# Kernel optimization log

Hardware: AMD Instinct MI355X
Metric: run time of the kernel (lower is better)

Reference implementation:

```python
import jax, jax.numpy as jnp
import numpy as np

N_NODES = 100000
N_EDGES = 3200000
HID = 52
N_LAYERS = 3


def setup_inputs() -> dict:
    key = jax.random.key(0)
    ks = jax.random.split(key, 6)
    x = jax.random.normal(ks[0], (N_NODES, HID), dtype=jnp.float32)
    edge_index = jax.random.randint(ks[1], (2, N_EDGES), 0, N_NODES, dtype=jnp.int32)
    w1 = jax.random.normal(ks[2], (N_LAYERS, HID, 2 * HID), dtype=jnp.float32) * 0.1
    b1 = jnp.zeros((N_LAYERS, 2 * HID), dtype=jnp.float32)
    w2 = jax.random.normal(ks[3], (N_LAYERS, 2 * HID, HID), dtype=jnp.float32) * 0.1
    b2 = jnp.zeros((N_LAYERS, HID), dtype=jnp.float32)
    eps = jnp.zeros((N_LAYERS,), dtype=jnp.float32)
    lin_w = jax.random.normal(ks[4], (HID * (N_LAYERS + 1), HID), dtype=jnp.float32) * 0.1
    lin_b = jnp.zeros((HID,), dtype=jnp.float32)
    return {"x": x, "edge_index": edge_index, "w1": w1, "b1": b1,
            "w2": w2, "b2": b2, "eps": eps, "lin_w": lin_w, "lin_b": lin_b}


def reference(x, edge_index, w1, b1, w2, b2, eps, lin_w, lin_b):
    src, dst = edge_index[0], edge_index[1]
    n = x.shape[0]
    h = x
    h_list = [x]
    for l in range(N_LAYERS):
        # GINConv: sum-aggregate neighbor features at target nodes
        agg = jax.ops.segment_sum(h[src], dst, num_segments=n)  # [N, HID]
        z = (1.0 + eps[l]) * h + agg
        # 2-layer MLP: Linear -> ReLU -> Linear
        z = jnp.maximum(z @ w1[l] + b1[l], 0.0) @ w2[l] + b2[l]
        # outer ReLU (dropout p=0 is identity)
        h = jnp.maximum(z, 0.0)
        h_list.append(h)
    node_repr = jnp.concatenate(h_list, axis=1)  # [N, HID*(L+1)]
    return node_repr @ lin_w + lin_b
```

## Files before the change

### kernel.cpp

```cpp
#include <hip/hip_runtime.h>

#define HID 52
#define HID2 104
#define P1_CHUNK 8192
#define NBIN_MAX 512
#define HSTRIDE 136
#define BINCAP 10240
#define SR_STRIDE 14336

typedef unsigned short ushort_t;
typedef unsigned int uint_t;
typedef short bf16x8 __attribute__((ext_vector_type(8)));
typedef float f32x4 __attribute__((ext_vector_type(4)));
typedef float f32x2 __attribute__((ext_vector_type(2)));

__device__ __forceinline__ ushort_t f2bf(float f) {
    union { float f; uint_t u; } c; c.f = f;
    uint_t u = c.u + 0x7FFFu + ((c.u >> 16) & 1u);
    return (ushort_t)(u >> 16);
}
__device__ __forceinline__ float bflo(uint_t u) {
    union { uint_t u; float f; } c; c.u = u << 16; return c.f;
}
__device__ __forceinline__ float bfhi(uint_t u) {
    union { uint_t u; float f; } c; c.u = u & 0xFFFF0000u; return c.f;
}
__device__ __forceinline__ f32x2 rawpair(uint_t a, uint_t b) {
    union { uint_t u; float f; } ca, cb; ca.u = a; cb.u = b;
    return (f32x2){ca.f, cb.f};
}
__device__ __forceinline__ f32x2 shlpair(uint_t a, uint_t b) {
    union { uint_t u; float f; } ca, cb; ca.u = a << 16; cb.u = b << 16;
    return (f32x2){ca.f, cb.f};
}
__device__ __forceinline__ void pkacc(f32x2& a, f32x2 b) {
    asm("v_pk_add_f32 %0, %0, %1" : "+v"(a) : "v"(b));
}
template<int IMM>
__device__ __forceinline__ f32x2 swz2(f32x2 v) {
    union { float f; int i; } a, b; a.f = v.x; b.f = v.y;
    int ra = __builtin_amdgcn_ds_swizzle(a.i, IMM);
    int rb = __builtin_amdgcn_ds_swizzle(b.i, IMM);
    union { int i; float f; } c, d; c.i = ra; d.i = rb;
    return (f32x2){c.f, d.f};
}

__global__ __launch_bounds__(512) void pass1_kernel(const int* __restrict__ src,
                                                    const int* __restrict__ dst,
                                                    int* __restrict__ gcnt,
                                                    uint_t* __restrict__ packed, int E) {
    __shared__ uint_t stage[P1_CHUNK];
    __shared__ ushort_t sbin[P1_CHUNK];
    __shared__ int cnt[NBIN_MAX];
    __shared__ int curs[NBIN_MAX];
    __shared__ int diff[NBIN_MAX];
    __shared__ int wsum[8];
    int tid = threadIdx.x;
    int lane = tid & 63, wv = tid >> 6;
    cnt[tid] = 0;
    __syncthreads();
    int base = blockIdx.x * P1_CHUNK;
    int cend = min(P1_CHUNK, E - base);
    int nq = cend >> 2;
    const uint4* d4p = (const uint4*)(dst + base);
    const uint4* s4p = (const uint4*)(src + base);
    for (int j = tid; j < nq; j += 512) {
        uint4 d = d4p[j];
        atomicAdd(&cnt[d.x >> 8], 1);
        atomicAdd(&cnt[d.y >> 8], 1);
        atomicAdd(&cnt[d.z >> 8], 1);
        atomicAdd(&cnt[d.w >> 8], 1);
    }
    for (int i = (nq << 2) + tid; i < cend; i += 512)
        atomicAdd(&cnt[((uint_t)dst[base + i]) >> 8], 1);
    __syncthreads();
    int c = cnt[tid];
    int inc = c;
#pragma unroll
    for (int off = 1; off < 64; off <<= 1) {
        int t = __shfl_up(inc, off);
        if (lane >= off) inc += t;
    }
    if (lane == 63) wsum[wv] = inc;
    __syncthreads();
    int wpre = 0;
#pragma unroll
    for (int i = 0; i < 7; i++) wpre += (i < wv) ? wsum[i] : 0;
    int ex = wpre + inc - c;
    curs[tid] = ex;
    int g = c ? (tid * BINCAP + atomicAdd(&gcnt[tid], c)) : 0;
    diff[tid] = g - ex;
    __syncthreads();
    for (int j = tid; j < nq; j += 512) {
        uint4 d = d4p[j];
        uint4 s = s4p[j];
        int b, pos;
        b = d.x >> 8; pos = atomicAdd(&curs[b], 1);
        stage[pos] = (s.x << 8) | (d.x & 255u); sbin[pos] = (ushort_t)b;
        b = d.y >> 8; pos = atomicAdd(&curs[b], 1);
        stage[pos] = (s.y << 8) | (d.y & 255u); sbin[pos] = (ushort_t)b;
        b = d.z >> 8; pos = atomicAdd(&curs[b], 1);
        stage[pos] = (s.z << 8) | (d.z & 255u); sbin[pos] = (ushort_t)b;
        b = d.w >> 8; pos = atomicAdd(&curs[b], 1);
        stage[pos] = (s.w << 8) | (d.w & 255u); sbin[pos] = (ushort_t)b;
    }
    for (int i = (nq << 2) + tid; i < cend; i += 512) {
        uint_t d = (uint_t)dst[base + i];
        uint_t s = (uint_t)src[base + i];
        int b = d >> 8;
        int pos = atomicAdd(&curs[b], 1);
        stage[pos] = (s << 8) | (d & 255u);
        sbin[pos] = (ushort_t)b;
    }
    __syncthreads();
    for (int i = tid; i < cend; i += 512) {
        packed[diff[sbin[i]] + i] = stage[i];
    }
}

__global__ __launch_bounds__(256) void mid_kernel(const uint_t* __restrict__ packed,
                                                  const int* __restrict__ gcnt,
                                                  int* __restrict__ srcsorted,
                                                  int* __restrict__ nrs,
                                                  int* __restrict__ ndeg,
                                                  const float* __restrict__ x,
                                                  const float* __restrict__ w1,
                                                  const float* __restrict__ w2,
                                                  const float* __restrict__ lin_w,
                                                  ushort_t* __restrict__ xb,
                                                  ushort_t* __restrict__ h1b,
                                                  ushort_t* __restrict__ h2b,
                                                  ushort_t* __restrict__ w1f,
                                                  ushort_t* __restrict__ w2f,
                                                  ushort_t* __restrict__ linf,
                                                  int N, int nbin, int nconv) {
    __shared__ int hist[256];
    __shared__ int curs[256];
    __shared__ int wsum[4];
    int blk = blockIdx.x;
    int tid = threadIdx.x;
    if (blk < nbin) {
        int b = blk;
        int lane = tid & 63, wv = tid >> 6;
        hist[tid] = 0;
        __syncthreads();
        int beg = b * BINCAP;
        int cntE = gcnt[b];
        int nq = cntE >> 2;
        const uint4* p4p = (const uint4*)(packed + beg);
        for (int j = tid; j < nq; j += 256) {
            uint4 p = p4p[j];
            atomicAdd(&hist[p.x & 255u], 1);
            atomicAdd(&hist[p.y & 255u], 1);
            atomicAdd(&hist[p.z & 255u], 1);
            atomicAdd(&hist[p.w & 255u], 1);
        }
        for (int i = (nq << 2) + tid; i < cntE; i += 256)
            atomicAdd(&hist[packed[beg + i] & 255u], 1);
        __syncthreads();
        int v = hist[tid];
        int pv = (v + 15) & ~15;
        int inc = pv;
#pragma unroll
        for (int off = 1; off < 64; off <<= 1) {
            int t = __shfl_up(inc, off);
            if (lane >= off) inc += t;
        }
        if (lane == 63) wsum[wv] = inc;
        __syncthreads();
        int wpre = 0;
#pragma unroll
        for (int i = 0; i < 3; i++) wpre += (i < wv) ? wsum[i] : 0;
        int start = b * SR_STRIDE + wpre + inc - pv;
        int node = b * 256 + tid;
        if (node < N) { nrs[node] = start; ndeg[node] = pv; }
        curs[tid] = start;
        __syncthreads();
        for (int j = tid; j < nq; j += 256) {
            uint4 p = p4p[j];
            int pos;
            pos = atomicAdd(&curs[p.x & 255u], 1); srcsorted[pos] = (int)(p.x >> 8);
            pos = atomicAdd(&curs[p.y & 255u], 1); srcsorted[pos] = (int)(p.y >> 8);
            pos = atomicAdd(&curs[p.z & 255u], 1); srcsorted[pos] = (int)(p.z >> 8);
            pos = atomicAdd(&curs[p.w & 255u], 1); srcsorted[pos] = (int)(p.w >> 8);
        }
        for (int i = (nq << 2) + tid; i < cntE; i += 256) {
            uint_t p = packed[beg + i];
            int pos = atomicAdd(&curs[p & 255u], 1);
            srcsorted[pos] = (int)(p >> 8);
        }
        __syncthreads();
        for (int i = start + v; i < start + pv; i++) srcsorted[i] = N;
        return;
    }
    if (blk < nbin + nconv) {
        int t = (blk - nbin) * 256 + tid;
        if (t >= N * 8) return;
        int node = t >> 3, pp = t & 7, c0 = pp * 8;
        uint4 u = make_uint4(0, 0, 0, 0);
        if (c0 < 48) {
            float4 xa = *(const float4*)(x + (size_t)node * HID + c0);
            float4 xc = *(const float4*)(x + (size_t)node * HID + c0 + 4);
            u.x = (uint_t)f2bf(xa.x) | ((uint_t)f2bf(xa.y) << 16);
            u.y = (uint_t)f2bf(xa.z) | ((uint_t)f2bf(xa.w) << 16);
            u.z = (uint_t)f2bf(xc.x) | ((uint_t)f2bf(xc.y) << 16);
            u.w = (uint_t)f2bf(xc.z) | ((uint_t)f2bf(xc.w) << 16);
        } else if (c0 == 48) {
            float4 xa = *(const float4*)(x + (size_t)node * HID + 48);
            u.x = (uint_t)f2bf(xa.x) | ((uint_t)f2bf(xa.y) << 16);
            u.y = (uint_t)f2bf(xa.z) | ((uint_t)f2bf(xa.w) << 16);
        }
        *(uint4*)(xb + (size_t)node * 64 + c0) = u;
        return;
    }
    if (blk == nbin + nconv) {
        ushort_t* arr = (tid < 64) ? xb : (tid < 128) ? h1b : h2b;
        arr[(size_t)N * 64 + (tid & 63)] = 0;
        return;
    }
    int gid = (blk - nbin - nconv - 1) * 4 + (tid >> 6);
    int lane = tid & 63;
    if (gid >= 122) return;
    int m = lane & 15, q = lane >> 4;
    ushort_t o[8];
    ushort_t* dstp;
    if (gid < 42) {
        int l = gid / 14, r = gid % 14, ct = r >> 1, ks = r & 1;
        int nn = ct * 16 + m;
#pragma unroll
        for (int j = 0; j < 8; j++) {
            int k = ks * 32 + q * 8 + j;
            o[j] = (k < HID && nn < HID2) ? f2bf(w1[((size_t)l * HID + k) * HID2 + nn]) : 0;
        }
        dstp = w1f + ((size_t)(l * 14 + ct * 2 + ks) * 64 + lane) * 8;
    } else if (gid < 90) {
        int g2 = gid - 42, l = g2 / 16, r = g2 % 16, ct = r >> 2, ks = r & 3;
        int nn = ct * 16 + m;
#pragma unroll
        for (int j = 0; j < 8; j++) {
            int k = ks * 32 + q * 8 + j;
            o[j] = (k < HID2 && nn < HID) ? f2bf(w2[((size_t)l * HID2 + k) * HID + nn]) : 0;
        }
        dstp = w2f + ((size_t)(l * 16 + ct * 4 + ks) * 64 + lane) * 8;
    } else {
        int g2 = gid - 90, ct = g2 >> 3, ks = g2 & 7;
        int nn = ct * 16 + m;
#pragma unroll
        for (int j = 0; j < 8; j++) {
            int kg = ks * 32 + q * 8 + j;
            int seg = kg >> 6, kk = kg & 63;
            o[j] = (kk < HID && nn < HID) ? f2bf(lin_w[((size_t)seg * HID + kk) * HID + nn]) : 0;
        }
        dstp = linf + ((size_t)(ct * 8 + ks) * 64 + lane) * 8;
    }
    uint4 u;
    u.x = (uint_t)o[0] | ((uint_t)o[1] << 16);
    u.y = (uint_t)o[2] | ((uint_t)o[3] << 16);
    u.z = (uint_t)o[4] | ((uint_t)o[5] << 16);
    u.w = (uint_t)o[6] | ((uint_t)o[7] << 16);
    *(uint4*)dstp = u;
}

__global__ __launch_bounds__(256) void agg_kernel(const ushort_t* __restrict__ hb,
                                                  const int* __restrict__ nrs,
                                                  const int* __restrict__ ndeg,
                                                  const int* __restrict__ srcsorted,
                                                  const float* __restrict__ eps,
                                                  ushort_t* __restrict__ zb, int n) {
    int wpair = (blockIdx.x * blockDim.x + threadIdx.x) >> 6;
    int lane = threadIdx.x & 63;
    int half = lane >> 5;
    int wid = wpair * 2 + half;
    bool valid = (wid < n);
    int node = valid ? wid : (n - 1);
    int hl = lane & 31;
    int g = hl >> 3;
    int sub = lane & 7;
    int beg = nrs[node];
    int total = valid ? ndeg[node] : 0;
    const char* hc = (const char*)hb;
    const char* sp = (const char*)srcsorted;
    unsigned lbB = (unsigned)sub * 16u;
    unsigned bo = (unsigned)(beg + g) * 4u;

    f32x2 AO0 = {0,0}, AO1 = {0,0}, AE0 = {0,0}, AE1 = {0,0};
    f32x2 BO0 = {0,0}, BO1 = {0,0}, BE0 = {0,0}, BE1 = {0,0};
    if (total > 0) {
        int f0 = *(const int*)(sp + bo);
        int f1 = *(const int*)(sp + bo + 16);
        int f2 = *(const int*)(sp + bo + 32);
        int f3 = *(const int*)(sp + bo + 48);
        int f4 = *(const int*)(sp + bo + 64);
        int f5 = *(const int*)(sp + bo + 80);
        int f6 = *(const int*)(sp + bo + 96);
        int f7 = *(const int*)(sp + bo + 112);
        for (int b = 0; b < total; b += 32) {
            bool ok = (b + 16) < total;
            int e0 = f0, e1 = f1, e2 = f2, e3 = f3;
            int e4 = ok ? f4 : n, e5 = ok ? f5 : n;
            int e6 = ok ? f6 : n, e7 = ok ? f7 : n;
            f0 = *(const int*)(sp + bo + 128);
            f1 = *(const int*)(sp + bo + 144);
            f2 = *(const int*)(sp + bo + 160);
            f3 = *(const int*)(sp + bo + 176);
            f4 = *(const int*)(sp + bo + 192);
            f5 = *(const int*)(sp + bo + 208);
            f6 = *(const int*)(sp + bo + 224);
            f7 = *(const int*)(sp + bo + 240);
            bo += 128;
            uint4 v0 = *(const uint4*)(hc + (((unsigned)e0 << 7) + lbB));
            uint4 v1 = *(const uint4*)(hc + (((unsigned)e1 << 7) + lbB));
            uint4 v2 = *(const uint4*)(hc + (((unsigned)e2 << 7) + lbB));
            uint4 v3 = *(const uint4*)(hc + (((unsigned)e3 << 7) + lbB));
            uint4 v4 = *(const uint4*)(hc + (((unsigned)e4 << 7) + lbB));
            uint4 v5 = *(const uint4*)(hc + (((unsigned)e5 << 7) + lbB));
            uint4 v6 = *(const uint4*)(hc + (((unsigned)e6 << 7) + lbB));
            uint4 v7 = *(const uint4*)(hc + (((unsigned)e7 << 7) + lbB));
            pkacc(AO0, rawpair(v0.x, v0.y)); pkacc(AO1, rawpair(v0.z, v0.w));
            pkacc(AE0, shlpair(v0.x, v0.y)); pkacc(AE1, shlpair(v0.z, v0.w));
            pkacc(BO0, rawpair(v1.x, v1.y)); pkacc(BO1, rawpair(v1.z, v1.w));
            pkacc(BE0, shlpair(v1.x, v1.y)); pkacc(BE1, shlpair(v1.z, v1.w));
            pkacc(AO0, rawpair(v2.x, v2.y)); pkacc(AO1, rawpair(v2.z, v2.w));
            pkacc(AE0, shlpair(v2.x, v2.y)); pkacc(AE1, shlpair(v2.z, v2.w));
            pkacc(BO0, rawpair(v3.x, v3.y)); pkacc(BO1, rawpair(v3.z, v3.w));
            pkacc(BE0, shlpair(v3.x, v3.y)); pkacc(BE1, shlpair(v3.z, v3.w));
            pkacc(AO0, rawpair(v4.x, v4.y)); pkacc(AO1, rawpair(v4.z, v4.w));
            pkacc(AE0, shlpair(v4.x, v4.y)); pkacc(AE1, shlpair(v4.z, v4.w));
            pkacc(BO0, rawpair(v5.x, v5.y)); pkacc(BO1, rawpair(v5.z, v5.w));
            pkacc(BE0, shlpair(v5.x, v5.y)); pkacc(BE1, shlpair(v5.z, v5.w));
            pkacc(AO0, rawpair(v6.x, v6.y)); pkacc(AO1, rawpair(v6.z, v6.w));
            pkacc(AE0, shlpair(v6.x, v6.y)); pkacc(AE1, shlpair(v6.z, v6.w));
            pkacc(BO0, rawpair(v7.x, v7.y)); pkacc(BO1, rawpair(v7.z, v7.w));
            pkacc(BE0, shlpair(v7.x, v7.y)); pkacc(BE1, shlpair(v7.z, v7.w));
        }
    }
    pkacc(AO0, BO0); pkacc(AO1, BO1);
    pkacc(AE0, BE0); pkacc(AE1, BE1);
    pkacc(AO0, swz2<0x201F>(AO0)); pkacc(AO1, swz2<0x201F>(AO1));
    pkacc(AE0, swz2<0x201F>(AE0)); pkacc(AE1, swz2<0x201F>(AE1));
    pkacc(AO0, swz2<0x401F>(AO0)); pkacc(AO1, swz2<0x401F>(AO1));
    pkacc(AE0, swz2<0x401F>(AE0)); pkacc(AE1, swz2<0x401F>(AE1));
    if (hl < 8 && valid) {
        float sc = 1.0f + eps[0];
        uint4 sv = *(const uint4*)(hb + (size_t)wid * 64 + hl * 8);
        float o0 = fmaf(sc, bflo(sv.x), AE0.x), o1 = fmaf(sc, bfhi(sv.x), AO0.x);
        float o2 = fmaf(sc, bflo(sv.y), AE0.y), o3 = fmaf(sc, bfhi(sv.y), AO0.y);
        float o4 = fmaf(sc, bflo(sv.z), AE1.x), o5 = fmaf(sc, bfhi(sv.z), AO1.x);
        float o6 = fmaf(sc, bflo(sv.w), AE1.y), o7 = fmaf(sc, bfhi(sv.w), AO1.y);
        uint4 u;
        u.x = (uint_t)f2bf(o0) | ((uint_t)f2bf(o1) << 16);
        u.y = (uint_t)f2bf(o2) | ((uint_t)f2bf(o3) << 16);
        u.z = (uint_t)f2bf(o4) | ((uint_t)f2bf(o5) << 16);
        u.w = (uint_t)f2bf(o6) | ((uint_t)f2bf(o7) << 16);
        *(uint4*)(zb + (size_t)wid * 64 + hl * 8) = u;
    }
}

template<int LAST>
__global__ __launch_bounds__(256) void mlp_kernel(const ushort_t* __restrict__ zb,
                                                  const ushort_t* __restrict__ w1f,
                                                  const float* __restrict__ b1,
                                                  const ushort_t* __restrict__ w2f,
                                                  const float* __restrict__ b2,
                                                  ushort_t* __restrict__ hbout,
                                                  const ushort_t* __restrict__ xb,
                                                  const ushort_t* __restrict__ h1b,
                                                  const ushort_t* __restrict__ h2b,
                                                  const ushort_t* __restrict__ linf,
                                                  const float* __restrict__ lin_b,
                                                  float* __restrict__ out, int n) {
    __shared__ ushort_t hid[64 * HSTRIDE];
    __shared__ ushort_t h3t[LAST ? 64 * 68 : 1];
    int tid = threadIdx.x;
    int w = tid >> 6, lane = tid & 63, m = lane & 15, q = lane >> 4;
    int nb = blockIdx.x * 64 + w * 16;
    int anode = min(nb + m, n - 1);
    bf16x8 afr[2];
    afr[0] = *(const bf16x8*)(zb + (size_t)anode * 64 + q * 8);
    afr[1] = *(const bf16x8*)(zb + (size_t)anode * 64 + 32 + q * 8);
    *(uint4*)((char*)hid + (size_t)(tid >> 2) * 272 + 208 + (size_t)(tid & 3) * 16)
        = make_uint4(0, 0, 0, 0);
    __syncthreads();

    f32x4 acc1[7];
#pragma unroll
    for (int ct = 0; ct < 7; ct++) {
        int col = ct * 16 + m;
        float bv = (col < HID2) ? b1[col] : 0.f;
        acc1[ct] = (f32x4){bv, bv, bv, bv};
    }
#pragma unroll
    for (int ks = 0; ks < 2; ks++) {
#pragma unroll
        for (int ct = 0; ct < 7; ct++) {
            bf16x8 b = *(const bf16x8*)(w1f + ((size_t)(ct * 2 + ks) * 64 + lane) * 8);
            acc1[ct] = __builtin_amdgcn_mfma_f32_16x16x32_bf16(afr[ks], b, acc1[ct], 0, 0, 0);
        }
    }
#pragma unroll
    for (int ct = 0; ct < 7; ct++) {
#pragma unroll
        for (int r = 0; r < 4; r++) {
            float v = fmaxf(acc1[ct][r], 0.f);
            int row = w * 16 + q * 4 + r;
            hid[row * HSTRIDE + ct * 16 + m] = f2bf(v);
        }
    }
    f32x4 acc2[4];
#pragma unroll
    for (int ct = 0; ct < 4; ct++) {
        int col = ct * 16 + m;
        float bv = (col < HID) ? b2[col] : 0.f;
        acc2[ct] = (f32x4){bv, bv, bv, bv};
    }
#pragma unroll
    for (int ks = 0; ks < 4; ks++) {
        bf16x8 a = *(const bf16x8*)&hid[(w * 16 + m) * HSTRIDE + ks * 32 + q * 8];
#pragma unroll
        for (int ct = 0; ct < 4; ct++) {
            bf16x8 b = *(const bf16x8*)(w2f + ((size_t)(ct * 4 + ks) * 64 + lane) * 8);
            acc2[ct] = __builtin_amdgcn_mfma_f32_16x16x32_bf16(a, b, acc2[ct], 0, 0, 0);
        }
    }

    if (!LAST) {
#pragma unroll
        for (int ct = 0; ct < 4; ct++) {
#pragma unroll
            for (int r = 0; r < 4; r++) {
                float v = fmaxf(acc2[ct][r], 0.f);
                hid[(w * 16 + q * 4 + r) * HSTRIDE + ct * 16 + m] = f2bf(v);
            }
        }
#pragma unroll
        for (int k = 0; k < 2; k++) {
            int c = lane + k * 64;
            int row = c >> 3, seg = c & 7;
            int node = nb + row;
            if (node < n) {
                uint4 v = *(const uint4*)&hid[(w * 16 + row) * HSTRIDE + seg * 8];
                *(uint4*)(hbout + (size_t)node * 64 + seg * 8) = v;
            }
        }
    } else {
#pragma unroll
        for (int ct = 0; ct < 4; ct++) {
#pragma unroll
            for (int r = 0; r < 4; r++) {
                float v = fmaxf(acc2[ct][r], 0.f);
                h3t[(w * 16 + q * 4 + r) * 68 + ct * 16 + m] = f2bf(v);
            }
        }
        f32x4 accF[4];
#pragma unroll
        for (int ct = 0; ct < 4; ct++) {
            int col = ct * 16 + m;
            float bv = (col < HID) ? lin_b[col] : 0.f;
            accF[ct] = (f32x4){bv, bv, bv, bv};
        }
        const ushort_t* segs[3] = {xb, h1b, h2b};
#pragma unroll
        for (int ks = 0; ks < 8; ks++) {
            bf16x8 a;
            if (ks < 6) {
                const ushort_t* p = segs[ks >> 1];
                a = *(const bf16x8*)(p + (size_t)anode * 64 + (ks & 1) * 32 + q * 8);
            } else {
                a = *(const bf16x8*)&h3t[(w * 16 + m) * 68 + (ks & 1) * 32 + q * 8];
            }
#pragma unroll
            for (int ct = 0; ct < 4; ct++) {
                bf16x8 b = *(const bf16x8*)(linf + ((size_t)(ct * 8 + ks) * 64 + lane) * 8);
                accF[ct] = __builtin_amdgcn_mfma_f32_16x16x32_bf16(a, b, accF[ct], 0, 0, 0);
            }
        }
#pragma unroll
        for (int ct = 0; ct < 4; ct++) {
            int col = ct * 16 + m;
            if (col < HID) {
#pragma unroll
                for (int r = 0; r < 4; r++) {
                    int node = nb + q * 4 + r;
                    if (node < n)
                        out[(size_t)node * HID + col] = accF[ct][r];
                }
            }
        }
    }
}

extern "C" void kernel_launch(void* const* d_in, const int* in_sizes, int n_in,
                              void* d_out, int out_size, void* d_ws, size_t ws_size,
                              hipStream_t stream) {
    const float* x     = (const float*)d_in[0];
    const int*   ei    = (const int*)d_in[1];
    const float* w1    = (const float*)d_in[2];
    const float* b1    = (const float*)d_in[3];
    const float* w2    = (const float*)d_in[4];
    const float* b2    = (const float*)d_in[5];
    const float* eps   = (const float*)d_in[6];
    const float* lin_w = (const float*)d_in[7];
    const float* lin_b = (const float*)d_in[8];
    float* out = (float*)d_out;

    const int N = in_sizes[0] / HID;
    const int E = in_sizes[1] / 2;
    const int* src = ei;
    const int* dst = ei + E;

    const int NBIN = (N + 255) / 256;

    char* p = (char*)d_ws;
    const size_t ROWS = (size_t)(N + 1) * 64 * 2;
    ushort_t* xb  = (ushort_t*)p;  p += ROWS;
    ushort_t* zb  = (ushort_t*)p;  p += ROWS;
    ushort_t* h1b = (ushort_t*)p;  p += ROWS;
    ushort_t* h2b = (ushort_t*)p;  p += ROWS;
    ushort_t* w1f = (ushort_t*)p;  p += 3 * 14 * 512 * 2;
    ushort_t* w2f = (ushort_t*)p;  p += 3 * 16 * 512 * 2;
    ushort_t* linf= (ushort_t*)p;  p += 32 * 512 * 2;
    int* gcnt     = (int*)p;       p += 512 * 4;
    int* nrs      = (int*)p;       p += (size_t)(N + 4) * 4;
    int* ndeg     = (int*)p;       p += (size_t)(N + 4) * 4;
    int* srcsorted = (int*)p;      p += (size_t)NBIN * SR_STRIDE * 4 + 256;
    uint_t* packed = (uint_t*)zb;

    ushort_t* hbs[3] = {xb, h1b, h2b};

    const int BLK = 256;
    const int NP1 = (E + P1_CHUNK - 1) / P1_CHUNK;
    const int NCONV = (N * 8 + BLK - 1) / BLK;
    const int NBUCK = (N + 63) / 64;
    const int NPAIR = (N + 1) / 2;
    dim3 blk(BLK);
    dim3 blk512(512);
    dim3 grid_agg(((size_t)NPAIR * 64 + BLK - 1) / BLK);

    hipMemsetAsync(gcnt, 0, 512 * sizeof(int), stream);
    pass1_kernel<<<NP1, blk512, 0, stream>>>(src, dst, gcnt, packed, E);
    mid_kernel<<<NBIN + NCONV + 1 + 31, blk, 0, stream>>>(packed, gcnt, srcsorted, nrs, ndeg,
                                                          x, w1, w2, lin_w,
                                                          xb, h1b, h2b,
                                                          w1f, w2f, linf,
                                                          N, NBIN, NCONV);

    for (int l = 0; l < 2; l++) {
        agg_kernel<<<grid_agg, blk, 0, stream>>>(hbs[l], nrs, ndeg, srcsorted, eps + l, zb, N);
        mlp_kernel<0><<<NBUCK, blk, 0, stream>>>(zb,
                                                 w1f + (size_t)l * 14 * 512,
                                                 b1 + (size_t)l * HID2,
                                                 w2f + (size_t)l * 16 * 512,
                                                 b2 + (size_t)l * HID,
                                                 hbs[l + 1],
                                                 nullptr, nullptr, nullptr,
                                                 nullptr, nullptr, nullptr, N);
    }
    agg_kernel<<<grid_agg, blk, 0, stream>>>(h2b, nrs, ndeg, srcsorted, eps + 2, zb, N);
    mlp_kernel<1><<<NBUCK, blk, 0, stream>>>(zb,
                                             w1f + 2 * 14 * 512,
                                             b1 + 2 * HID2,
                                             w2f + 2 * 16 * 512,
                                             b2 + 2 * HID,
                                             nullptr,
                                             xb, h1b, h2b,
                                             linf, lin_b, out, N);
}
```

Measured before the change: 331.4 us.

## Fuse all GIN layers into one persistent cooperative kernel with grid barriers

Replaces the six per-layer aggregation and MLP launches with a single cooperative persistent kernel. Waves loop over node pairs and MLP buckets grid-stride, and layers are separated by atomic-counter grid barriers. This removes five kernel launches and the gaps between them, and the aggregation loop prefetches the next node's edge indices. In exchange, each barrier costs some spin-waiting, the grid is capped at the occupancy limit, and the code falls back to the old launches if a cooperative launch is unavailable.

```diff
diff --git a/kernel.cpp b/kernel.cpp
--- a/kernel.cpp
+++ b/kernel.cpp
@@ -489,6 +489,273 @@
     }
 }
 
+__device__ __forceinline__ void gridbar(int* bar, int nblk, int ph) {
+    __syncthreads();
+    __threadfence();
+    if (threadIdx.x == 0) {
+        atomicAdd(&bar[ph], 1);
+        while (__hip_atomic_load(&bar[ph], __ATOMIC_RELAXED, __HIP_MEMORY_SCOPE_AGENT) < nblk)
+            __builtin_amdgcn_s_sleep(2);
+    }
+    __syncthreads();
+    __threadfence();
+}
+
+__global__ __launch_bounds__(256) void layers_kernel(
+        const int* __restrict__ nrs, const int* __restrict__ ndeg,
+        const int* __restrict__ srcsorted, const float* __restrict__ eps,
+        const ushort_t* __restrict__ w1f0, const float* __restrict__ b10,
+        const ushort_t* __restrict__ w2f0, const float* __restrict__ b20,
+        ushort_t* __restrict__ xb, ushort_t* __restrict__ zb,
+        ushort_t* __restrict__ h1b, ushort_t* __restrict__ h2b,
+        const ushort_t* __restrict__ linf, const float* __restrict__ lin_b,
+        float* __restrict__ out, int* __restrict__ bar, int nblocks, int n) {
+    __shared__ ushort_t hid[64 * HSTRIDE];
+    int tid = threadIdx.x;
+    int w = tid >> 6, lane = tid & 63, m = lane & 15, q = lane >> 4;
+    int half = lane >> 5, hl = lane & 31, g = hl >> 3, sub = lane & 7;
+    *(uint4*)((char*)hid + (size_t)(tid >> 2) * 272 + 208 + (size_t)(tid & 3) * 16)
+        = make_uint4(0, 0, 0, 0);
+
+    const char* sp = (const char*)srcsorted;
+    unsigned lbB = (unsigned)sub * 16u;
+    int NPAIRv = (n + 1) >> 1;
+    int NBUCKv = (n + 63) >> 6;
+    int totalWaves = nblocks * 4;
+    int wgid = blockIdx.x * 4 + w;
+
+    const ushort_t* hbs_[3] = {xb, h1b, h2b};
+    ushort_t* hout_[2] = {h1b, h2b};
+
+    for (int l = 0; l < 3; l++) {
+        const ushort_t* hb = hbs_[l];
+        const char* hc = (const char*)hb;
+        float sc = 1.0f + eps[l];
+
+        int u = wgid;
+        int beg = 0, total = 0;
+        int f0 = 0, f1 = 0, f2 = 0, f3 = 0, f4 = 0, f5 = 0, f6 = 0, f7 = 0;
+        if (u < NPAIRv) {
+            int wid0 = u * 2 + half;
+            bool v0 = (wid0 < n);
+            int node0 = v0 ? wid0 : (n - 1);
+            beg = nrs[node0];
+            total = v0 ? ndeg[node0] : 0;
+            unsigned b0o = (unsigned)(beg + g) * 4u;
+            f0 = *(const int*)(sp + b0o);       f1 = *(const int*)(sp + b0o + 16);
+            f2 = *(const int*)(sp + b0o + 32);  f3 = *(const int*)(sp + b0o + 48);
+            f4 = *(const int*)(sp + b0o + 64);  f5 = *(const int*)(sp + b0o + 80);
+            f6 = *(const int*)(sp + b0o + 96);  f7 = *(const int*)(sp + b0o + 112);
+        }
+        while (u < NPAIRv) {
+            int widc = u * 2 + half;
+            bool validc = (widc < n);
+            int un = u + totalWaves;
+            int nwid = un * 2 + half;
+            bool nvalid = (un < NPAIRv) && (nwid < n);
+            int nnode = nvalid ? nwid : (n - 1);
+            int nbeg = nrs[nnode];
+            int ntotal = nvalid ? ndeg[nnode] : 0;
+
+            unsigned bo = (unsigned)(beg + g) * 4u;
+            f32x2 AO0 = {0,0}, AO1 = {0,0}, AE0 = {0,0}, AE1 = {0,0};
+            f32x2 BO0 = {0,0}, BO1 = {0,0}, BE0 = {0,0}, BE1 = {0,0};
+            if (total > 0) {
+                for (int b = 0; b < total; b += 32) {
+                    bool ok = (b + 16) < total;
+                    int e0 = f0, e1 = f1, e2 = f2, e3 = f3;
+                    int e4 = ok ? f4 : n, e5 = ok ? f5 : n;
+                    int e6 = ok ? f6 : n, e7 = ok ? f7 : n;
+                    f0 = *(const int*)(sp + bo + 128);
+                    f1 = *(const int*)(sp + bo + 144);
+                    f2 = *(const int*)(sp + bo + 160);
+                    f3 = *(const int*)(sp + bo + 176);
+                    f4 = *(const int*)(sp + bo + 192);
+                    f5 = *(const int*)(sp + bo + 208);
+                    f6 = *(const int*)(sp + bo + 224);
+                    f7 = *(const int*)(sp + bo + 240);
+                    bo += 128;
+                    uint4 v0 = *(const uint4*)(hc + (((unsigned)e0 << 7) + lbB));
+                    uint4 v1 = *(const uint4*)(hc + (((unsigned)e1 << 7) + lbB));
+                    uint4 v2 = *(const uint4*)(hc + (((unsigned)e2 << 7) + lbB));
+                    uint4 v3 = *(const uint4*)(hc + (((unsigned)e3 << 7) + lbB));
+                    uint4 v4 = *(const uint4*)(hc + (((unsigned)e4 << 7) + lbB));
+                    uint4 v5 = *(const uint4*)(hc + (((unsigned)e5 << 7) + lbB));
+                    uint4 v6 = *(const uint4*)(hc + (((unsigned)e6 << 7) + lbB));
+                    uint4 v7 = *(const uint4*)(hc + (((unsigned)e7 << 7) + lbB));
+                    pkacc(AO0, rawpair(v0.x, v0.y)); pkacc(AO1, rawpair(v0.z, v0.w));
+                    pkacc(AE0, shlpair(v0.x, v0.y)); pkacc(AE1, shlpair(v0.z, v0.w));
+                    pkacc(BO0, rawpair(v1.x, v1.y)); pkacc(BO1, rawpair(v1.z, v1.w));
+                    pkacc(BE0, shlpair(v1.x, v1.y)); pkacc(BE1, shlpair(v1.z, v1.w));
+                    pkacc(AO0, rawpair(v2.x, v2.y)); pkacc(AO1, rawpair(v2.z, v2.w));
+                    pkacc(AE0, shlpair(v2.x, v2.y)); pkacc(AE1, shlpair(v2.z, v2.w));
+                    pkacc(BO0, rawpair(v3.x, v3.y)); pkacc(BO1, rawpair(v3.z, v3.w));
+                    pkacc(BE0, shlpair(v3.x, v3.y)); pkacc(BE1, shlpair(v3.z, v3.w));
+                    pkacc(AO0, rawpair(v4.x, v4.y)); pkacc(AO1, rawpair(v4.z, v4.w));
+                    pkacc(AE0, shlpair(v4.x, v4.y)); pkacc(AE1, shlpair(v4.z, v4.w));
+                    pkacc(BO0, rawpair(v5.x, v5.y)); pkacc(BO1, rawpair(v5.z, v5.w));
+                    pkacc(BE0, shlpair(v5.x, v5.y)); pkacc(BE1, shlpair(v5.z, v5.w));
+                    pkacc(AO0, rawpair(v6.x, v6.y)); pkacc(AO1, rawpair(v6.z, v6.w));
+                    pkacc(AE0, shlpair(v6.x, v6.y)); pkacc(AE1, shlpair(v6.z, v6.w));
+                    pkacc(BO0, rawpair(v7.x, v7.y)); pkacc(BO1, rawpair(v7.z, v7.w));
+                    pkacc(BE0, shlpair(v7.x, v7.y)); pkacc(BE1, shlpair(v7.z, v7.w));
+                }
+            }
+            unsigned nbo = (unsigned)(nbeg + g) * 4u;
+            int nf0 = *(const int*)(sp + nbo);       int nf1 = *(const int*)(sp + nbo + 16);
+            int nf2 = *(const int*)(sp + nbo + 32);  int nf3 = *(const int*)(sp + nbo + 48);
+            int nf4 = *(const int*)(sp + nbo + 64);  int nf5 = *(const int*)(sp + nbo + 80);
+            int nf6 = *(const int*)(sp + nbo + 96);  int nf7 = *(const int*)(sp + nbo + 112);
+
+            pkacc(AO0, BO0); pkacc(AO1, BO1);
+            pkacc(AE0, BE0); pkacc(AE1, BE1);
+            pkacc(AO0, swz2<0x201F>(AO0)); pkacc(AO1, swz2<0x201F>(AO1));
+            pkacc(AE0, swz2<0x201F>(AE0)); pkacc(AE1, swz2<0x201F>(AE1));
+            pkacc(AO0, swz2<0x401F>(AO0)); pkacc(AO1, swz2<0x401F>(AO1));
+            pkacc(AE0, swz2<0x401F>(AE0)); pkacc(AE1, swz2<0x401F>(AE1));
+            if (hl < 8 && validc) {
+                uint4 sv = *(const uint4*)(hb + (size_t)widc * 64 + hl * 8);
+                float o0 = fmaf(sc, bflo(sv.x), AE0.x), o1 = fmaf(sc, bfhi(sv.x), AO0.x);
+                float o2 = fmaf(sc, bflo(sv.y), AE0.y), o3 = fmaf(sc, bfhi(sv.y), AO0.y);
+                float o4 = fmaf(sc, bflo(sv.z), AE1.x), o5 = fmaf(sc, bfhi(sv.z), AO1.x);
+                float o6 = fmaf(sc, bflo(sv.w), AE1.y), o7 = fmaf(sc, bfhi(sv.w), AO1.y);
+                uint4 uo;
+                uo.x = (uint_t)f2bf(o0) | ((uint_t)f2bf(o1) << 16);
+                uo.y = (uint_t)f2bf(o2) | ((uint_t)f2bf(o3) << 16);
+                uo.z = (uint_t)f2bf(o4) | ((uint_t)f2bf(o5) << 16);
+                uo.w = (uint_t)f2bf(o6) | ((uint_t)f2bf(o7) << 16);
+                *(uint4*)(zb + (size_t)widc * 64 + hl * 8) = uo;
+            }
+            u = un; beg = nbeg; total = ntotal;
+            f0 = nf0; f1 = nf1; f2 = nf2; f3 = nf3;
+            f4 = nf4; f5 = nf5; f6 = nf6; f7 = nf7;
+        }
+        gridbar(bar, nblocks, 2 * l);
+
+        const ushort_t* w1f = w1f0 + (size_t)l * 14 * 512;
+        const float* b1v = b10 + (size_t)l * HID2;
+        const ushort_t* w2f = w2f0 + (size_t)l * 16 * 512;
+        const float* b2v = b20 + (size_t)l * HID;
+        bool LASTl = (l == 2);
+        for (int vb = blockIdx.x; vb < NBUCKv; vb += nblocks) {
+            int nb = vb * 64 + w * 16;
+            int anode = min(nb + m, n - 1);
+            bf16x8 afr[2];
+            afr[0] = *(const bf16x8*)(zb + (size_t)anode * 64 + q * 8);
+            afr[1] = *(const bf16x8*)(zb + (size_t)anode * 64 + 32 + q * 8);
+
+            f32x4 acc1[7];
+#pragma unroll
+            for (int ct = 0; ct < 7; ct++) {
+                int col = ct * 16 + m;
+                float bv = (col < HID2) ? b1v[col] : 0.f;
+                acc1[ct] = (f32x4){bv, bv, bv, bv};
+            }
+#pragma unroll
+            for (int ks = 0; ks < 2; ks++) {
+#pragma unroll
+                for (int ct = 0; ct < 7; ct++) {
+                    bf16x8 b = *(const bf16x8*)(w1f + ((size_t)(ct * 2 + ks) * 64 + lane) * 8);
+                    acc1[ct] = __builtin_amdgcn_mfma_f32_16x16x32_bf16(afr[ks], b, acc1[ct], 0, 0, 0);
+                }
+            }
+#pragma unroll
+            for (int ct = 0; ct < 7; ct++) {
+#pragma unroll
+                for (int r = 0; r < 4; r++) {
+                    float v = fmaxf(acc1[ct][r], 0.f);
+                    int row = w * 16 + q * 4 + r;
+                    hid[row * HSTRIDE + ct * 16 + m] = f2bf(v);
+                }
+            }
+            f32x4 acc2[4];
+#pragma unroll
+            for (int ct = 0; ct < 4; ct++) {
+                int col = ct * 16 + m;
+                float bv = (col < HID) ? b2v[col] : 0.f;
+                acc2[ct] = (f32x4){bv, bv, bv, bv};
+            }
+#pragma unroll
+            for (int ks = 0; ks < 4; ks++) {
+                bf16x8 a = *(const bf16x8*)&hid[(w * 16 + m) * HSTRIDE + ks * 32 + q * 8];
+#pragma unroll
+                for (int ct = 0; ct < 4; ct++) {
+                    bf16x8 b = *(const bf16x8*)(w2f + ((size_t)(ct * 4 + ks) * 64 + lane) * 8);
+                    acc2[ct] = __builtin_amdgcn_mfma_f32_16x16x32_bf16(a, b, acc2[ct], 0, 0, 0);
+                }
+            }
+
+            if (!LASTl) {
+#pragma unroll
+                for (int ct = 0; ct < 4; ct++) {
+#pragma unroll
+                    for (int r = 0; r < 4; r++) {
+                        float v = fmaxf(acc2[ct][r], 0.f);
+                        hid[(w * 16 + q * 4 + r) * HSTRIDE + ct * 16 + m] = f2bf(v);
+                    }
+                }
+                ushort_t* hout = hout_[l];
+#pragma unroll
+                for (int k = 0; k < 2; k++) {
+                    int cidx = lane + k * 64;
+                    int row = cidx >> 3, seg = cidx & 7;
+                    int node = nb + row;
+                    if (node < n) {
+                        uint4 v = *(const uint4*)&hid[(w * 16 + row) * HSTRIDE + seg * 8];
+                        *(uint4*)(hout + (size_t)node * 64 + seg * 8) = v;
+                    }
+                }
+            } else {
+                ushort_t* h3w = hid + (size_t)w * 16 * HSTRIDE;
+#pragma unroll
+                for (int ct = 0; ct < 4; ct++) {
+#pragma unroll
+                    for (int r = 0; r < 4; r++) {
+                        float v = fmaxf(acc2[ct][r], 0.f);
+                        h3w[(q * 4 + r) * 68 + ct * 16 + m] = f2bf(v);
+                    }
+                }
+                f32x4 accF[4];
+#pragma unroll
+                for (int ct = 0; ct < 4; ct++) {
+                    int col = ct * 16 + m;
+                    float bv = (col < HID) ? lin_b[col] : 0.f;
+                    accF[ct] = (f32x4){bv, bv, bv, bv};
+                }
+                const ushort_t* segs[3] = {xb, h1b, h2b};
+#pragma unroll
+                for (int ks = 0; ks < 8; ks++) {
+                    bf16x8 a;
+                    if (ks < 6) {
+                        const ushort_t* p = segs[ks >> 1];
+                        a = *(const bf16x8*)(p + (size_t)anode * 64 + (ks & 1) * 32 + q * 8);
+                    } else {
+                        a = *(const bf16x8*)&h3w[m * 68 + (ks & 1) * 32 + q * 8];
+                    }
+#pragma unroll
+                    for (int ct = 0; ct < 4; ct++) {
+                        bf16x8 b = *(const bf16x8*)(linf + ((size_t)(ct * 8 + ks) * 64 + lane) * 8);
+                        accF[ct] = __builtin_amdgcn_mfma_f32_16x16x32_bf16(a, b, accF[ct], 0, 0, 0);
+                    }
+                }
+#pragma unroll
+                for (int ct = 0; ct < 4; ct++) {
+                    int col = ct * 16 + m;
+                    if (col < HID) {
+#pragma unroll
+                        for (int r = 0; r < 4; r++) {
+                            int node = nb + q * 4 + r;
+                            if (node < n)
+                                out[(size_t)node * HID + col] = accF[ct][r];
+                        }
+                    }
+                }
+            }
+        }
+        if (l < 2) gridbar(bar, nblocks, 2 * l + 1);
+    }
+}
+
 extern "C" void kernel_launch(void* const* d_in, const int* in_sizes, int n_in,
                               void* d_out, int out_size, void* d_ws, size_t ws_size,
                               hipStream_t stream) {
@@ -520,6 +787,7 @@
     ushort_t* w2f = (ushort_t*)p;  p += 3 * 16 * 512 * 2;
     ushort_t* linf= (ushort_t*)p;  p += 32 * 512 * 2;
     int* gcnt     = (int*)p;       p += 512 * 4;
+    int* bar      = (int*)p;       p += 8 * 4;
     int* nrs      = (int*)p;       p += (size_t)(N + 4) * 4;
     int* ndeg     = (int*)p;       p += (size_t)(N + 4) * 4;
     int* srcsorted = (int*)p;      p += (size_t)NBIN * SR_STRIDE * 4 + 256;
@@ -536,7 +804,7 @@
     dim3 blk512(512);
     dim3 grid_agg(((size_t)NPAIR * 64 + BLK - 1) / BLK);
 
-    hipMemsetAsync(gcnt, 0, 512 * sizeof(int), stream);
+    hipMemsetAsync(gcnt, 0, (512 + 8) * sizeof(int), stream);
     pass1_kernel<<<NP1, blk512, 0, stream>>>(src, dst, gcnt, packed, E);
     mid_kernel<<<NBIN + NCONV + 1 + 31, blk, 0, stream>>>(packed, gcnt, srcsorted, nrs, ndeg,
                                                           x, w1, w2, lin_w,
@@ -544,24 +812,52 @@
                                                           w1f, w2f, linf,
                                                           N, NBIN, NCONV);
 
-    for (int l = 0; l < 2; l++) {
-        agg_kernel<<<grid_agg, blk, 0, stream>>>(hbs[l], nrs, ndeg, srcsorted, eps + l, zb, N);
-        mlp_kernel<0><<<NBUCK, blk, 0, stream>>>(zb,
-                                                 w1f + (size_t)l * 14 * 512,
-                                                 b1 + (size_t)l * HID2,
-                                                 w2f + (size_t)l * 16 * 512,
-                                                 b2 + (size_t)l * HID,
-                                                 hbs[l + 1],
-                                                 nullptr, nullptr, nullptr,
-                                                 nullptr, nullptr, nullptr, N);
-    }
-    agg_kernel<<<grid_agg, blk, 0, stream>>>(h2b, nrs, ndeg, srcsorted, eps + 2, zb, N);
-    mlp_kernel<1><<<NBUCK, blk, 0, stream>>>(zb,
-                                             w1f + 2 * 14 * 512,
-                                             b1 + 2 * HID2,
-                                             w2f + 2 * 16 * 512,
-                                             b2 + 2 * HID,
-                                             nullptr,
-                                             xb, h1b, h2b,
-                                             linf, lin_b, out, N);
-}
+    bool coop_ok = false;
+    int dev = 0;
+    hipGetDevice(&dev);
+    int coop_attr = 0;
+    hipDeviceGetAttribute(&coop_attr, hipDeviceAttributeCooperativeLaunch, dev);
+    if (coop_attr) {
+        int occ = 0;
+        hipError_t oe = hipOccupancyMaxActiveBlocksPerMultiprocessor(&occ, layers_kernel, BLK, 0);
+        int cus = 0;
+        hipDeviceGetAttribute(&cus, hipDeviceAttributeMultiprocessorCount, dev);
+        if (cus <= 0) cus = 256;
+        if (oe == hipSuccess && occ >= 1) {
+            int nblocks = occ * cus;
+            if (nblocks > 2048) nblocks = 2048;
+            void* args[] = {
+                (void*)&nrs, (void*)&ndeg, (void*)&srcsorted, (void*)&eps,
+                (void*)&w1f, (void*)&b1, (void*)&w2f, (void*)&b2,
+                (void*)&xb, (void*)&zb, (void*)&h1b, (void*)&h2b,
+                (void*)&linf, (void*)&lin_b, (void*)&out,
+                (void*)&bar, (void*)&nblocks, (void*)&N
+            };
+            hipError_t le = hipLaunchCooperativeKernel((const void*)layers_kernel,
+                                                       dim3(nblocks), blk, args, 0, stream);
+            coop_ok = (le == hipSuccess);
+        }
+    }
+    if (!coop_ok) {
+        for (int l = 0; l < 2; l++) {
+            agg_kernel<<<grid_agg, blk, 0, stream>>>(hbs[l], nrs, ndeg, srcsorted, eps + l, zb, N);
+            mlp_kernel<0><<<NBUCK, blk, 0, stream>>>(zb,
+                                                     w1f + (size_t)l * 14 * 512,
+                                                     b1 + (size_t)l * HID2,
+                                                     w2f + (size_t)l * 16 * 512,
+                                                     b2 + (size_t)l * HID,
+                                                     hbs[l + 1],
+                                                     nullptr, nullptr, nullptr,
+                                                     nullptr, nullptr, nullptr, N);
+        }
+        agg_kernel<<<grid_agg, blk, 0, stream>>>(h2b, nrs, ndeg, srcsorted, eps + 2, zb, N);
+        mlp_kernel<1><<<NBUCK, blk, 0, stream>>>(zb,
+                                                 w1f + 2 * 14 * 512,
+                                                 b1 + 2 * HID2,
+                                                 w2f + 2 * 16 * 512,
+                                                 b2 + 2 * HID,
+                                                 nullptr,
+                                                 xb, h1b, h2b,
+                                                 linf, lin_b, out, N);
+    }
+}
```

Result: no change. 329.4 us (-0.6%).

## Split neighbor aggregation into four feature-slice blocks with sliced z layout

Applied to the files above, without the earlier changes.

The aggregation kernel now gives each 256-thread block one 32-byte feature quarter of four nodes, so the block grid is four times larger. Each wave handles one node with 32 edges in flight, each edge gathered by two lanes. The intermediate z buffer becomes four separate slices so each quarter is written contiguously, and the MLP kernel reads its A fragments from these slices. The goal is to keep each concurrent gather working on a narrower column slice for better L2 locality and more parallelism. The cost is a longer cross-lane reduction and extra index loads, since each edge index is fetched once per quarter.

```diff
diff --git a/kernel.cpp b/kernel.cpp
--- a/kernel.cpp
+++ b/kernel.cpp
@@ -43,6 +43,12 @@
     int rb = __builtin_amdgcn_ds_swizzle(b.i, IMM);
     union { int i; float f; } c, d; c.i = ra; d.i = rb;
     return (f32x2){c.f, d.f};
+}
+__device__ __forceinline__ f32x2 sh32(f32x2 v) {
+    f32x2 r;
+    r.x = __shfl_xor(v.x, 32);
+    r.y = __shfl_xor(v.y, 32);
+    return r;
 }
 
 __global__ __launch_bounds__(512) void pass1_kernel(const int* __restrict__ src,
@@ -261,88 +267,54 @@
     *(uint4*)dstp = u;
 }
 
-__global__ __launch_bounds__(256) void agg_kernel(const ushort_t* __restrict__ hb,
-                                                  const int* __restrict__ nrs,
-                                                  const int* __restrict__ ndeg,
-                                                  const int* __restrict__ srcsorted,
-                                                  const float* __restrict__ eps,
-                                                  ushort_t* __restrict__ zb, int n) {
-    int wpair = (blockIdx.x * blockDim.x + threadIdx.x) >> 6;
-    int lane = threadIdx.x & 63;
-    int half = lane >> 5;
-    int wid = wpair * 2 + half;
-    bool valid = (wid < n);
-    int node = valid ? wid : (n - 1);
-    int hl = lane & 31;
-    int g = hl >> 3;
-    int sub = lane & 7;
-    int beg = nrs[node];
-    int total = valid ? ndeg[node] : 0;
+__global__ __launch_bounds__(256) void agg4_kernel(const ushort_t* __restrict__ hb,
+                                                   const int* __restrict__ nrs,
+                                                   const int* __restrict__ ndeg,
+                                                   const int* __restrict__ srcsorted,
+                                                   const float* __restrict__ eps,
+                                                   ushort_t* __restrict__ zbq,
+                                                   int n, int slstride) {
+    int q = blockIdx.x & 3;
+    int nodeg = blockIdx.x >> 2;
+    int tid = threadIdx.x;
+    int w = tid >> 6, lane = tid & 63;
+    int node = nodeg * 4 + w;
+    bool valid = (node < n);
+    int nd = valid ? node : (n - 1);
+    int e = lane >> 1, s = lane & 1;
+    int beg = nrs[nd];
+    int total = valid ? ndeg[nd] : 0;
     const char* hc = (const char*)hb;
     const char* sp = (const char*)srcsorted;
-    unsigned lbB = (unsigned)sub * 16u;
-    unsigned bo = (unsigned)(beg + g) * 4u;
+    unsigned lq = (unsigned)(q * 32 + s * 16);
 
     f32x2 AO0 = {0,0}, AO1 = {0,0}, AE0 = {0,0}, AE1 = {0,0};
-    f32x2 BO0 = {0,0}, BO1 = {0,0}, BE0 = {0,0}, BE1 = {0,0};
     if (total > 0) {
-        int f0 = *(const int*)(sp + bo);
-        int f1 = *(const int*)(sp + bo + 16);
-        int f2 = *(const int*)(sp + bo + 32);
-        int f3 = *(const int*)(sp + bo + 48);
-        int f4 = *(const int*)(sp + bo + 64);
-        int f5 = *(const int*)(sp + bo + 80);
-        int f6 = *(const int*)(sp + bo + 96);
-        int f7 = *(const int*)(sp + bo + 112);
+        unsigned bo = (unsigned)(beg + e) * 4u;
+        int f = *(const int*)(sp + bo);
         for (int b = 0; b < total; b += 32) {
-            bool ok = (b + 16) < total;
-            int e0 = f0, e1 = f1, e2 = f2, e3 = f3;
-            int e4 = ok ? f4 : n, e5 = ok ? f5 : n;
-            int e6 = ok ? f6 : n, e7 = ok ? f7 : n;
-            f0 = *(const int*)(sp + bo + 128);
-            f1 = *(const int*)(sp + bo + 144);
-            f2 = *(const int*)(sp + bo + 160);
-            f3 = *(const int*)(sp + bo + 176);
-            f4 = *(const int*)(sp + bo + 192);
-            f5 = *(const int*)(sp + bo + 208);
-            f6 = *(const int*)(sp + bo + 224);
-            f7 = *(const int*)(sp + bo + 240);
+            bool ok = (e < 16) | ((b + 16) < total);
+            int e0 = ok ? f : n;
+            f = *(const int*)(sp + bo + 128);
             bo += 128;
-            uint4 v0 = *(const uint4*)(hc + (((unsigned)e0 << 7) + lbB));
-            uint4 v1 = *(const uint4*)(hc + (((unsigned)e1 << 7) + lbB));
-            uint4 v2 = *(const uint4*)(hc + (((unsigned)e2 << 7) + lbB));
-            uint4 v3 = *(const uint4*)(hc + (((unsigned)e3 << 7) + lbB));
-            uint4 v4 = *(const uint4*)(hc + (((unsigned)e4 << 7) + lbB));
-            uint4 v5 = *(const uint4*)(hc + (((unsigned)e5 << 7) + lbB));
-            uint4 v6 = *(const uint4*)(hc + (((unsigned)e6 << 7) + lbB));
-            uint4 v7 = *(const uint4*)(hc + (((unsigned)e7 << 7) + lbB));
-            pkacc(AO0, rawpair(v0.x, v0.y)); pkacc(AO1, rawpair(v0.z, v0.w));
-            pkacc(AE0, shlpair(v0.x, v0.y)); pkacc(AE1, shlpair(v0.z, v0.w));
-            pkacc(BO0, rawpair(v1.x, v1.y)); pkacc(BO1, rawpair(v1.z, v1.w));
-            pkacc(BE0, shlpair(v1.x, v1.y)); pkacc(BE1, shlpair(v1.z, v1.w));
-            pkacc(AO0, rawpair(v2.x, v2.y)); pkacc(AO1, rawpair(v2.z, v2.w));
-            pkacc(AE0, shlpair(v2.x, v2.y)); pkacc(AE1, shlpair(v2.z, v2.w));
-            pkacc(BO0, rawpair(v3.x, v3.y)); pkacc(BO1, rawpair(v3.z, v3.w));
-            pkacc(BE0, shlpair(v3.x, v3.y)); pkacc(BE1, shlpair(v3.z, v3.w));
-            pkacc(AO0, rawpair(v4.x, v4.y)); pkacc(AO1, rawpair(v4.z, v4.w));
-            pkacc(AE0, shlpair(v4.x, v4.y)); pkacc(AE1, shlpair(v4.z, v4.w));
-            pkacc(BO0, rawpair(v5.x, v5.y)); pkacc(BO1, rawpair(v5.z, v5.w));
-            pkacc(BE0, shlpair(v5.x, v5.y)); pkacc(BE1, shlpair(v5.z, v5.w));
-            pkacc(AO0, rawpair(v6.x, v6.y)); pkacc(AO1, rawpair(v6.z, v6.w));
-            pkacc(AE0, shlpair(v6.x, v6.y)); pkacc(AE1, shlpair(v6.z, v6.w));
-            pkacc(BO0, rawpair(v7.x, v7.y)); pkacc(BO1, rawpair(v7.z, v7.w));
-            pkacc(BE0, shlpair(v7.x, v7.y)); pkacc(BE1, shlpair(v7.z, v7.w));
-        }
-    }
-    pkacc(AO0, BO0); pkacc(AO1, BO1);
-    pkacc(AE0, BE0); pkacc(AE1, BE1);
+            uint4 v = *(const uint4*)(hc + (((unsigned)e0 << 7) + lq));
+            pkacc(AO0, rawpair(v.x, v.y)); pkacc(AO1, rawpair(v.z, v.w));
+            pkacc(AE0, shlpair(v.x, v.y)); pkacc(AE1, shlpair(v.z, v.w));
+        }
+    }
+    pkacc(AO0, swz2<0x081F>(AO0)); pkacc(AO1, swz2<0x081F>(AO1));
+    pkacc(AE0, swz2<0x081F>(AE0)); pkacc(AE1, swz2<0x081F>(AE1));
+    pkacc(AO0, swz2<0x101F>(AO0)); pkacc(AO1, swz2<0x101F>(AO1));
+    pkacc(AE0, swz2<0x101F>(AE0)); pkacc(AE1, swz2<0x101F>(AE1));
     pkacc(AO0, swz2<0x201F>(AO0)); pkacc(AO1, swz2<0x201F>(AO1));
     pkacc(AE0, swz2<0x201F>(AE0)); pkacc(AE1, swz2<0x201F>(AE1));
     pkacc(AO0, swz2<0x401F>(AO0)); pkacc(AO1, swz2<0x401F>(AO1));
     pkacc(AE0, swz2<0x401F>(AE0)); pkacc(AE1, swz2<0x401F>(AE1));
-    if (hl < 8 && valid) {
+    pkacc(AO0, sh32(AO0)); pkacc(AO1, sh32(AO1));
+    pkacc(AE0, sh32(AE0)); pkacc(AE1, sh32(AE1));
+    if (lane < 2 && valid) {
         float sc = 1.0f + eps[0];
-        uint4 sv = *(const uint4*)(hb + (size_t)wid * 64 + hl * 8);
+        uint4 sv = *(const uint4*)(hb + (size_t)node * 64 + q * 16 + s * 8);
         float o0 = fmaf(sc, bflo(sv.x), AE0.x), o1 = fmaf(sc, bfhi(sv.x), AO0.x);
         float o2 = fmaf(sc, bflo(sv.y), AE0.y), o3 = fmaf(sc, bfhi(sv.y), AO0.y);
         float o4 = fmaf(sc, bflo(sv.z), AE1.x), o5 = fmaf(sc, bfhi(sv.z), AO1.x);
@@ -352,12 +324,12 @@
         u.y = (uint_t)f2bf(o2) | ((uint_t)f2bf(o3) << 16);
         u.z = (uint_t)f2bf(o4) | ((uint_t)f2bf(o5) << 16);
         u.w = (uint_t)f2bf(o6) | ((uint_t)f2bf(o7) << 16);
-        *(uint4*)(zb + (size_t)wid * 64 + hl * 8) = u;
+        *(uint4*)(zbq + (size_t)q * slstride + (size_t)node * 16 + s * 8) = u;
     }
 }
 
 template<int LAST>
-__global__ __launch_bounds__(256) void mlp_kernel(const ushort_t* __restrict__ zb,
+__global__ __launch_bounds__(256) void mlp_kernel(const ushort_t* __restrict__ zbq,
                                                   const ushort_t* __restrict__ w1f,
                                                   const float* __restrict__ b1,
                                                   const ushort_t* __restrict__ w2f,
@@ -368,7 +340,7 @@
                                                   const ushort_t* __restrict__ h2b,
                                                   const ushort_t* __restrict__ linf,
                                                   const float* __restrict__ lin_b,
-                                                  float* __restrict__ out, int n) {
+                                                  float* __restrict__ out, int n, int slstride) {
     __shared__ ushort_t hid[64 * HSTRIDE];
     __shared__ ushort_t h3t[LAST ? 64 * 68 : 1];
     int tid = threadIdx.x;
@@ -376,8 +348,11 @@
     int nb = blockIdx.x * 64 + w * 16;
     int anode = min(nb + m, n - 1);
     bf16x8 afr[2];
-    afr[0] = *(const bf16x8*)(zb + (size_t)anode * 64 + q * 8);
-    afr[1] = *(const bf16x8*)(zb + (size_t)anode * 64 + 32 + q * 8);
+#pragma unroll
+    for (int ks = 0; ks < 2; ks++) {
+        int qq = ks * 2 + (q >> 1), ss = q & 1;
+        afr[ks] = *(const bf16x8*)(zbq + (size_t)qq * slstride + (size_t)anode * 16 + ss * 8);
+    }
     *(uint4*)((char*)hid + (size_t)(tid >> 2) * 272 + 208 + (size_t)(tid & 3) * 16)
         = make_uint4(0, 0, 0, 0);
     __syncthreads();
@@ -513,7 +488,7 @@
     char* p = (char*)d_ws;
     const size_t ROWS = (size_t)(N + 1) * 64 * 2;
     ushort_t* xb  = (ushort_t*)p;  p += ROWS;
-    ushort_t* zb  = (ushort_t*)p;  p += ROWS;
+    ushort_t* zbq = (ushort_t*)p;  p += ROWS;
     ushort_t* h1b = (ushort_t*)p;  p += ROWS;
     ushort_t* h2b = (ushort_t*)p;  p += ROWS;
     ushort_t* w1f = (ushort_t*)p;  p += 3 * 14 * 512 * 2;
@@ -523,7 +498,7 @@
     int* nrs      = (int*)p;       p += (size_t)(N + 4) * 4;
     int* ndeg     = (int*)p;       p += (size_t)(N + 4) * 4;
     int* srcsorted = (int*)p;      p += (size_t)NBIN * SR_STRIDE * 4 + 256;
-    uint_t* packed = (uint_t*)zb;
+    uint_t* packed = (uint_t*)zbq;
 
     ushort_t* hbs[3] = {xb, h1b, h2b};
 
@@ -531,10 +506,11 @@
     const int NP1 = (E + P1_CHUNK - 1) / P1_CHUNK;
     const int NCONV = (N * 8 + BLK - 1) / BLK;
     const int NBUCK = (N + 63) / 64;
-    const int NPAIR = (N + 1) / 2;
+    const int NB4 = (N + 3) / 4;
+    const int SLSTRIDE = NB4 * 4 * 16;
     dim3 blk(BLK);
     dim3 blk512(512);
-    dim3 grid_agg(((size_t)NPAIR * 64 + BLK - 1) / BLK);
+    dim3 grid_agg4((size_t)NB4 * 4);
 
     hipMemsetAsync(gcnt, 0, 512 * sizeof(int), stream);
     pass1_kernel<<<NP1, blk512, 0, stream>>>(src, dst, gcnt, packed, E);
@@ -545,23 +521,25 @@
                                                           N, NBIN, NCONV);
 
     for (int l = 0; l < 2; l++) {
-        agg_kernel<<<grid_agg, blk, 0, stream>>>(hbs[l], nrs, ndeg, srcsorted, eps + l, zb, N);
-        mlp_kernel<0><<<NBUCK, blk, 0, stream>>>(zb,
+        agg4_kernel<<<grid_agg4, blk, 0, stream>>>(hbs[l], nrs, ndeg, srcsorted, eps + l,
+                                                   zbq, N, SLSTRIDE);
+        mlp_kernel<0><<<NBUCK, blk, 0, stream>>>(zbq,
                                                  w1f + (size_t)l * 14 * 512,
                                                  b1 + (size_t)l * HID2,
                                                  w2f + (size_t)l * 16 * 512,
                                                  b2 + (size_t)l * HID,
                                                  hbs[l + 1],
                                                  nullptr, nullptr, nullptr,
-                                                 nullptr, nullptr, nullptr, N);
-    }
-    agg_kernel<<<grid_agg, blk, 0, stream>>>(h2b, nrs, ndeg, srcsorted, eps + 2, zb, N);
-    mlp_kernel<1><<<NBUCK, blk, 0, stream>>>(zb,
+                                                 nullptr, nullptr, nullptr, N, SLSTRIDE);
+    }
+    agg4_kernel<<<grid_agg4, blk, 0, stream>>>(h2b, nrs, ndeg, srcsorted, eps + 2,
+                                               zbq, N, SLSTRIDE);
+    mlp_kernel<1><<<NBUCK, blk, 0, stream>>>(zbq,
                                              w1f + 2 * 14 * 512,
                                              b1 + 2 * HID2,
                                              w2f + 2 * 16 * 512,
                                              b2 + 2 * HID,
                                              nullptr,
                                              xb, h1b, h2b,
-                                             linf, lin_b, out, N);
-}
+                                             linf, lin_b, out, N, SLSTRIDE);
+}
```

Measured after the change: 732.8 us. 121% more time.
